# Performance work log

Measured on AMD Instinct MI355X. Metric: run time of the kernel, lower is better.

The kernel has to match this reference:

```python
import jax, jax.numpy as jnp
import numpy as np

EMBED_DIM = 256
NUM_HEADS = 8
HEAD_DIM = EMBED_DIM // NUM_HEADS
WINDOW = 31
B, S = 4, 2048


def _make_params(key):
    ks = jax.random.split(key, 8)
    sc = 0.05
    Wq = jax.random.normal(ks[0], (NUM_HEADS, EMBED_DIM, HEAD_DIM), jnp.float32) * sc
    bq = jax.random.normal(ks[1], (NUM_HEADS, HEAD_DIM), jnp.float32) * sc
    Wk = jax.random.normal(ks[2], (NUM_HEADS, EMBED_DIM, HEAD_DIM), jnp.float32) * sc
    bk = jax.random.normal(ks[3], (NUM_HEADS, HEAD_DIM), jnp.float32) * sc
    Wv = jax.random.normal(ks[4], (NUM_HEADS, EMBED_DIM, HEAD_DIM), jnp.float32) * sc
    bv = jax.random.normal(ks[5], (NUM_HEADS, HEAD_DIM), jnp.float32) * sc
    Wo = jax.random.normal(ks[6], (NUM_HEADS * HEAD_DIM, EMBED_DIM), jnp.float32) * sc
    bo = jax.random.normal(ks[7], (EMBED_DIM,), jnp.float32) * sc
    return Wq, bq, Wk, bk, Wv, bv, Wo, bo


def setup_inputs() -> dict:
    key = jax.random.key(0)
    k1, k2, k3, k4 = jax.random.split(key, 4)
    eeg = jax.random.normal(k1, (B, S, EMBED_DIM), jnp.float32)
    pps = jax.random.normal(k2, (B, S, EMBED_DIM), jnp.float32)
    e2p = _make_params(k3)
    p2e = _make_params(k4)
    names = ["Wq", "bq", "Wk", "bk", "Wv", "bv", "Wo", "bo"]
    inp = {"eeg": eeg, "pps": pps}
    for n, p in zip(names, e2p):
        inp["e2p_" + n] = p
    for n, p in zip(names, p2e):
        inp["p2e_" + n] = p
    return inp


def _cross_window_attn(q_seq, kv_seq, Wq, bq, Wk, bk, Wv, bv, Wo, bo, window):
    # q_seq, kv_seq: [B, S, D]. Each query position i attends to window of
    # the zero-padded kv sequence centered at i (pad positions get bias-only k/v,
    # matching torch Linear applied to zero vectors).
    b, s, d_in = q_seq.shape
    h, _, hd = Wq.shape
    pad = (window - 1) // 2
    kv_pad = jnp.pad(kv_seq, ((0, 0), (pad, pad), (0, 0)))
    Q = jnp.einsum('bsd,hde->bhse', q_seq, Wq) + bq[None, :, None, :]
    K = jnp.einsum('bsd,hde->bhse', kv_pad, Wk) + bk[None, :, None, :]
    V = jnp.einsum('bsd,hde->bhse', kv_pad, Wv) + bv[None, :, None, :]
    idx = jnp.arange(s)[:, None] + jnp.arange(window)[None, :]  # [S, W]
    Kw = K[:, :, idx, :]  # [B, H, S, W, hd]
    Vw = V[:, :, idx, :]
    scores = jnp.einsum('bhse,bhswe->bhsw', Q, Kw) / np.sqrt(hd).astype(np.float32)
    attn = jax.nn.softmax(scores, axis=-1)
    out = jnp.einsum('bhsw,bhswe->bhse', attn, Vw)  # [B, H, S, hd]
    out = out.transpose(0, 2, 1, 3).reshape(b, s, h * hd)
    return out @ Wo + bo


def reference(eeg, pps,
              e2p_Wq, e2p_bq, e2p_Wk, e2p_bk, e2p_Wv, e2p_bv, e2p_Wo, e2p_bo,
              p2e_Wq, p2e_bq, p2e_Wk, p2e_bk, p2e_Wv, p2e_bv, p2e_Wo, p2e_bo):
    fused_eeg = _cross_window_attn(eeg, pps, e2p_Wq, e2p_bq, e2p_Wk, e2p_bk,
                                   e2p_Wv, e2p_bv, e2p_Wo, e2p_bo, WINDOW)
    fused_pps = _cross_window_attn(pps, eeg, p2e_Wq, p2e_bq, p2e_Wk, p2e_bk,
                                   p2e_Wv, p2e_bv, p2e_Wo, p2e_bo, WINDOW)
    return fused_eeg, fused_pps
```

## Files before the change

kernel.cpp:

```cpp
#include <hip/hip_runtime.h>

static __device__ __forceinline__ float bf2f(unsigned short u) {
    return __uint_as_float(((unsigned int)u) << 16);
}
static __device__ __forceinline__ unsigned short f2bf(float f) {
    unsigned int x = __float_as_uint(f);
    unsigned int lsb = (x >> 16) & 1u;
    x += 0x7fffu + lsb;
    return (unsigned short)(x >> 16);
}

typedef __attribute__((ext_vector_type(8))) short short8;
typedef __attribute__((ext_vector_type(4))) float floatx4;

static __device__ __forceinline__ short8 ldg8(const unsigned short* p) {
    short8 v; __builtin_memcpy(&v, p, 16); return v;
}


__global__ __launch_bounds__(256) void repack_kernel(
    const float* e2p_Wq, const float* e2p_bq,
    const float* e2p_Wk, const float* e2p_bk,
    const float* e2p_Wv, const float* e2p_bv,
    const float* e2p_Wo, const float* e2p_bo,
    const float* p2e_Wq, const float* p2e_bq,
    const float* p2e_Wk, const float* p2e_bk,
    const float* p2e_Wv, const float* p2e_bv,
    const float* p2e_Wo, const float* p2e_bo,
    const float* eeg, const float* pps,
    unsigned short* Wpack, unsigned short* Wopack, float* bias_pack, float* bias2,
    unsigned short* Abf)
{
    const int idx = blockIdx.x * 256 + threadIdx.x;

    if (idx < 49152) {
        int inp = idx / 24576, r = idx % 24576;
        int n = r >> 5, k8 = r & 31;
        int kc = k8 >> 2, q4 = k8 & 3, kb = k8 * 8;
        int proj = n / 256, h = (n % 256) / 32, e = n % 32;
        const float* W;
        if (inp == 0) W = (proj == 0) ? e2p_Wq : (proj == 1) ? p2e_Wk : p2e_Wv;
        else          W = (proj == 0) ? p2e_Wq : (proj == 1) ? e2p_Wk : e2p_Wv;
        unsigned short o[8];
        #pragma unroll
        for (int j = 0; j < 8; ++j) o[j] = f2bf(W[h * 8192 + (kb + j) * 32 + e]);
        __builtin_memcpy(Wpack + inp * 196608 + ((n >> 4) * 8 + kc) * 512 + (q4 * 16 + (n & 15)) * 8, o, 16);
    }
    int i2 = idx - 49152;
    if (i2 >= 0 && i2 < 16384) {
        int dir = i2 / 8192, r = i2 % 8192;
        int n = r >> 5, k8 = r & 31;
        int kc = k8 >> 2, q4 = k8 & 3, kb = k8 * 8;
        const float* Wo = dir ? p2e_Wo : e2p_Wo;
        unsigned short o[8];
        #pragma unroll
        for (int j = 0; j < 8; ++j) o[j] = f2bf(Wo[(kb + j) * 256 + n]);
        __builtin_memcpy(Wopack + dir * 65536 + ((n >> 4) * 8 + kc) * 512 + (q4 * 16 + (n & 15)) * 8, o, 16);
    }
    if (idx < 1536) {
        int inp = idx / 768, n = idx % 768;
        int proj = n / 256, he = n % 256;
        const float* bsrc;
        if (inp == 0) bsrc = (proj == 0) ? e2p_bq : (proj == 1) ? p2e_bk : p2e_bv;
        else          bsrc = (proj == 0) ? p2e_bq : (proj == 1) ? e2p_bk : e2p_bv;
        bias_pack[idx] = bsrc[he];
    }
    if (idx >= 1536 && idx < 2048) {
        int j = idx - 1536;
        int dir = j / 256, n = j % 256;
        bias2[j] = (dir == 0 ? e2p_bo : p2e_bo)[n];
    }
    {
        int m_total = idx >> 5;
        int k8 = idx & 31;
        int inp = m_total >> 13, m = m_total & 8191;
        int kc = k8 >> 2, q4 = k8 & 3, kb = k8 * 8;
        const float* src = inp ? pps : eeg;
        float v[8];
        __builtin_memcpy(v, src + (long)m * 256 + kb, 32);
        unsigned short o[8];
        #pragma unroll
        for (int j = 0; j < 8; ++j) o[j] = f2bf(v[j]);
        __builtin_memcpy(Abf + inp * 2097152 + (((m >> 4) * 8 + kc) * 512 + (q4 * 16 + (m & 15)) * 8), o, 16);
    }
}

__global__ __launch_bounds__(256) void mfma_gemm_kernel(
    const unsigned short* __restrict__ A0, const unsigned short* __restrict__ A1,
    const unsigned short* __restrict__ B0f, const unsigned short* __restrict__ B1f,
    const float* __restrict__ bias0, const float* __restrict__ bias1,
    unsigned short* __restrict__ C0, unsigned short* __restrict__ C1,
    int N)
{
    __shared__ __align__(16) unsigned short Cs[128][136];

    const int z = blockIdx.z;
    const unsigned short* A = z ? A1 : A0;
    const unsigned short* Bf = z ? B1f : B0f;
    const float* bias = z ? bias1 : bias0;
    unsigned short* C = z ? C1 : C0;

    const int tid = threadIdx.x;
    const long m0 = (long)blockIdx.x * 128;
    const int n0 = blockIdx.y * 128;

    const int lane = tid & 63;
    const int wv = tid >> 6;
    const int wm = (wv >> 1) * 64, wn = (wv & 1) * 64;
    const int fr = lane & 15, q4 = lane >> 4;

    const unsigned short* Aw = A + ((blockIdx.x * 8 + (wm >> 4)) * 8) * 512 + lane * 8;
    const unsigned short* Bw = Bf + ((blockIdx.y * 8 + (wn >> 4)) * 8) * 512 + lane * 8;

    floatx4 acc[4][4] = {};
    short8 af[2][4], bf_[2][4];

    #pragma unroll
    for (int i = 0; i < 4; ++i) af[0][i] = ldg8(Aw + i * 4096);
    #pragma unroll
    for (int j = 0; j < 4; ++j) bf_[0][j] = ldg8(Bw + j * 4096);

    #pragma unroll
    for (int kc = 0; kc < 8; ++kc) {
        const int cur = kc & 1, nxt = cur ^ 1;
        if (kc < 7) {
            #pragma unroll
            for (int i = 0; i < 4; ++i) af[nxt][i] = ldg8(Aw + (i * 8 + kc + 1) * 512);
            #pragma unroll
            for (int j = 0; j < 4; ++j) bf_[nxt][j] = ldg8(Bw + (j * 8 + kc + 1) * 512);
        }
        #pragma unroll
        for (int i = 0; i < 4; ++i)
            #pragma unroll
            for (int j = 0; j < 4; ++j)
                acc[i][j] = __builtin_amdgcn_mfma_f32_16x16x32_bf16(af[cur][i], bf_[cur][j], acc[i][j], 0, 0, 0);
    }

    float bj[4];
    #pragma unroll
    for (int j = 0; j < 4; ++j) bj[j] = bias[n0 + wn + j * 16 + fr];

    const int cr0 = wm + (q4 << 2);
    #pragma unroll
    for (int i = 0; i < 4; ++i)
        #pragma unroll
        for (int j = 0; j < 4; ++j)
            #pragma unroll
            for (int r = 0; r < 4; ++r)
                Cs[cr0 + i * 16 + r][wn + j * 16 + fr] = f2bf(acc[i][j][r] + bj[j]);
    __syncthreads();

    const int rr = tid >> 4, cc = (tid & 15) * 8;
    #pragma unroll
    for (int p = 0; p < 8; ++p) {
        int r = p * 16 + rr;
        unsigned short tmp[8];
        __builtin_memcpy(tmp, &Cs[r][cc], 16);
        __builtin_memcpy(C + (m0 + r) * N + n0 + cc, tmp, 16);
    }
}

#define KROWS 48
#define VROWS 64
#define KVSTR 264
__global__ __launch_bounds__(512) void attn_out_kernel(
    const unsigned short* __restrict__ Y, const float* __restrict__ bias_pack,
    const unsigned short* __restrict__ Wopack, const float* __restrict__ bias2,
    float* __restrict__ out)
{
    __shared__ unsigned short smem[(KROWS + VROWS) * KVSTR];
    unsigned short* Ks = smem;
    unsigned short* Vs = smem + KROWS * KVSTR;
    unsigned short (*Ps)[16][72] = (unsigned short(*)[16][72])smem;
    unsigned short (*As)[KVSTR] = (unsigned short(*)[KVSTR])smem;

    const int s0 = blockIdx.x * 16;
    const int b = blockIdx.y, dir = blockIdx.z;
    const int kvinp = 1 - dir;
    const int tid = threadIdx.x;

    const float* bkv = bias_pack + kvinp * 768;
    const long kvbase = ((long)kvinp * 8192 + b * 2048) * 768;

    {
        const int r = tid >> 3, seg = (tid & 7) * 32;
        int p = s0 - 15 + r;
        unsigned short vr[32];
        if (p >= 0 && p < 2048) {
            __builtin_memcpy(vr, Y + kvbase + (long)p * 768 + 512 + seg, 64);
        } else {
            #pragma unroll
            for (int j = 0; j < 32; ++j) vr[j] = f2bf(bkv[512 + seg + j]);
        }
        __builtin_memcpy(&Vs[r * KVSTR + seg], vr, 64);
        if (tid < 384) {
            unsigned short kr[32];
            if (p >= 0 && p < 2048) {
                __builtin_memcpy(kr, Y + kvbase + (long)p * 768 + 256 + seg, 64);
            } else {
                #pragma unroll
                for (int j = 0; j < 32; ++j) kr[j] = f2bf(bkv[256 + seg + j]);
            }
            __builtin_memcpy(&Ks[r * KVSTR + seg], kr, 64);
        }
    }

    const int lane = tid & 63;
    const int wv = tid >> 6;
    const int fr = lane & 15, q4 = lane >> 4;
    short8 aq = ldg8(Y + ((long)dir * 8192 + b * 2048 + s0 + fr) * 768 + wv * 32 + q4 * 8);

    __syncthreads();

    floatx4 sacc[3] = {};
    #pragma unroll
    for (int kvt = 0; kvt < 3; ++kvt) {
        short8 bk_ = *(const short8*)&Ks[(kvt * 16 + fr) * KVSTR + wv * 32 + q4 * 8];
        sacc[kvt] = __builtin_amdgcn_mfma_f32_16x16x32_bf16(aq, bk_, sacc[kvt], 0, 0, 0);
    }

    float sv[3][4];
    float mx[4] = {-3.0e38f, -3.0e38f, -3.0e38f, -3.0e38f};
    #pragma unroll
    for (int kvt = 0; kvt < 3; ++kvt)
        #pragma unroll
        for (int reg = 0; reg < 4; ++reg) {
            int i = q4 * 4 + reg;
            int jc = kvt * 16 + fr;
            int d = jc - i;
            float x = (d >= 0 && d <= 30) ? sacc[kvt][reg] * 0.17677669529663687f : -3.0e38f;
            sv[kvt][reg] = x;
            mx[reg] = fmaxf(mx[reg], x);
        }
    #pragma unroll
    for (int off = 1; off < 16; off <<= 1)
        #pragma unroll
        for (int reg = 0; reg < 4; ++reg)
            mx[reg] = fmaxf(mx[reg], __shfl_xor(mx[reg], off));
    float ps[4] = {};
    #pragma unroll
    for (int kvt = 0; kvt < 3; ++kvt)
        #pragma unroll
        for (int reg = 0; reg < 4; ++reg) {
            float e = __expf(sv[kvt][reg] - mx[reg]);
            sv[kvt][reg] = e;
            ps[reg] += e;
        }
    #pragma unroll
    for (int off = 1; off < 16; off <<= 1)
        #pragma unroll
        for (int reg = 0; reg < 4; ++reg)
            ps[reg] += __shfl_xor(ps[reg], off);

    __syncthreads();

    #pragma unroll
    for (int reg = 0; reg < 4; ++reg) {
        int i = q4 * 4 + reg;
        #pragma unroll
        for (int kvt = 0; kvt < 3; ++kvt)
            Ps[wv][i][kvt * 16 + fr] = f2bf(sv[kvt][reg]);
        Ps[wv][i][48 + fr] = 0;
    }

    floatx4 oacc[2] = {};
    #pragma unroll
    for (int ch = 0; ch < 2; ++ch) {
        short8 ap = *(const short8*)&Ps[wv][fr][ch * 32 + q4 * 8];
        #pragma unroll
        for (int et = 0; et < 2; ++et) {
            short8 bv;
            #pragma unroll
            for (int j = 0; j < 8; ++j)
                bv[j] = (short)Vs[(ch * 32 + q4 * 8 + j) * KVSTR + wv * 32 + et * 16 + fr];
            oacc[et] = __builtin_amdgcn_mfma_f32_16x16x32_bf16(ap, bv, oacc[et], 0, 0, 0);
        }
    }

    float rs[4];
    #pragma unroll
    for (int reg = 0; reg < 4; ++reg) rs[reg] = 1.0f / ps[reg];

    __syncthreads();

    #pragma unroll
    for (int et = 0; et < 2; ++et)
        #pragma unroll
        for (int reg = 0; reg < 4; ++reg)
            As[q4 * 4 + reg][wv * 32 + et * 16 + fr] = f2bf(oacc[et][reg] * rs[reg]);

    __syncthreads();

    const unsigned short* Wo = Wopack + dir * 65536 + lane * 8;
    const int nw = wv * 32;
    floatx4 oa[2] = {};
    #pragma unroll
    for (int kc = 0; kc < 8; ++kc) {
        short8 ap = *(const short8*)&As[fr][kc * 32 + q4 * 8];
        #pragma unroll
        for (int j = 0; j < 2; ++j) {
            short8 bw = ldg8(Wo + ((wv * 2 + j) * 8 + kc) * 512);
            oa[j] = __builtin_amdgcn_mfma_f32_16x16x32_bf16(ap, bw, oa[j], 0, 0, 0);
        }
    }

    float bj[2];
    #pragma unroll
    for (int j = 0; j < 2; ++j) bj[j] = bias2[dir * 256 + nw + j * 16 + fr];

    float* outp = out + (long)dir * 2097152;
    #pragma unroll
    for (int j = 0; j < 2; ++j)
        #pragma unroll
        for (int reg = 0; reg < 4; ++reg) {
            int i = q4 * 4 + reg;
            outp[((long)b * 2048 + s0 + i) * 256 + nw + j * 16 + fr] = oa[j][reg] + bj[j];
        }
}

extern "C" void kernel_launch(void* const* d_in, const int* in_sizes, int n_in,
                              void* d_out, int out_size, void* d_ws, size_t ws_size,
                              hipStream_t stream)
{
    float* out = (float*)d_out;

    char* ws = (char*)d_ws;
    unsigned short* Wpack   = (unsigned short*)(ws + 0);
    unsigned short* Wopack  = (unsigned short*)(ws + 786432);
    float*          biasP   = (float*)(ws + 1048576);
    float*          bias2   = (float*)(ws + 1054720);
    unsigned short* Y       = (unsigned short*)(ws + 1056768);
    unsigned short* Abf     = (unsigned short*)(ws + 26222592);

    repack_kernel<<<2048, 256, 0, stream>>>(
        (const float*)d_in[2],  (const float*)d_in[3],
        (const float*)d_in[4],  (const float*)d_in[5],
        (const float*)d_in[6],  (const float*)d_in[7],
        (const float*)d_in[8],  (const float*)d_in[9],
        (const float*)d_in[10], (const float*)d_in[11],
        (const float*)d_in[12], (const float*)d_in[13],
        (const float*)d_in[14], (const float*)d_in[15],
        (const float*)d_in[16], (const float*)d_in[17],
        (const float*)d_in[0],  (const float*)d_in[1],
        Wpack, Wopack, biasP, bias2, Abf);

    mfma_gemm_kernel<<<dim3(64, 6, 2), 256, 0, stream>>>(
        Abf, Abf + 2097152, Wpack, Wpack + 196608, biasP, biasP + 768,
        Y, Y + 8192 * 768, 768);

    attn_out_kernel<<<dim3(128, 4, 2), 512, 0, stream>>>(Y, biasP, Wopack, bias2, out);
}
```

Measured before the change: 140.4 us.

## Coalesce repack and output stores via shared-memory staging and block role split

The repack kernel now assigns dedicated block ranges to each task. The activation conversion stages each 16-row tile through shared memory, so the packed bf16 layout is written as contiguous 16-byte chunks instead of scattered stores. The weight repack index mapping is reordered so consecutive threads write adjacent packed addresses. The attention output epilogue stages the fp32 result tile in shared memory and writes full 32-byte row segments, replacing strided per-element stores, at the cost of extra barriers and shared-memory traffic.

```diff
diff --git a/kernel.cpp b/kernel.cpp
--- a/kernel.cpp
+++ b/kernel.cpp
@@ -31,11 +31,33 @@
     unsigned short* Wpack, unsigned short* Wopack, float* bias_pack, float* bias2,
     unsigned short* Abf)
 {
-    const int idx = blockIdx.x * 256 + threadIdx.x;
-
-    if (idx < 49152) {
+    __shared__ unsigned short tr[2048];
+    const int bid = blockIdx.x, tid = threadIdx.x;
+
+    if (bid < 2048) {
+        const int g = bid >> 1, kc_half = (bid & 1) * 4;
+        const int inp = g >> 9;
+        const int m = (g & 511) * 16 + (tid >> 4);
+        const int k8 = kc_half * 4 + (tid & 15);
+        const float* src = inp ? pps : eeg;
+        float v[8];
+        __builtin_memcpy(v, src + (long)m * 256 + k8 * 8, 32);
+        unsigned short o[8];
+        #pragma unroll
+        for (int j = 0; j < 8; ++j) o[j] = f2bf(v[j]);
+        const int k8l = tid & 15;
+        __builtin_memcpy(&tr[(k8l >> 2) * 512 + ((k8l & 3) * 16 + (tid >> 4)) * 8], o, 16);
+        __syncthreads();
+        unsigned short t[8];
+        __builtin_memcpy(t, &tr[tid * 8], 16);
+        __builtin_memcpy(Abf + inp * 2097152 + ((g & 511) * 8 + kc_half) * 512 + tid * 8, t, 16);
+        return;
+    }
+    if (bid < 2240) {
+        int idx = (bid - 2048) * 256 + tid;
         int inp = idx / 24576, r = idx % 24576;
-        int n = r >> 5, k8 = r & 31;
+        int n = (r & 15) | ((r >> 9) << 4);
+        int k8 = (r >> 4) & 31;
         int kc = k8 >> 2, q4 = k8 & 3, kb = k8 * 8;
         int proj = n / 256, h = (n % 256) / 32, e = n % 32;
         const float* W;
@@ -45,43 +67,35 @@
         #pragma unroll
         for (int j = 0; j < 8; ++j) o[j] = f2bf(W[h * 8192 + (kb + j) * 32 + e]);
         __builtin_memcpy(Wpack + inp * 196608 + ((n >> 4) * 8 + kc) * 512 + (q4 * 16 + (n & 15)) * 8, o, 16);
-    }
-    int i2 = idx - 49152;
-    if (i2 >= 0 && i2 < 16384) {
+        return;
+    }
+    if (bid < 2304) {
+        int i2 = (bid - 2240) * 256 + tid;
         int dir = i2 / 8192, r = i2 % 8192;
-        int n = r >> 5, k8 = r & 31;
+        int n = (r & 15) | ((r >> 9) << 4);
+        int k8 = (r >> 4) & 31;
         int kc = k8 >> 2, q4 = k8 & 3, kb = k8 * 8;
         const float* Wo = dir ? p2e_Wo : e2p_Wo;
         unsigned short o[8];
         #pragma unroll
         for (int j = 0; j < 8; ++j) o[j] = f2bf(Wo[(kb + j) * 256 + n]);
         __builtin_memcpy(Wopack + dir * 65536 + ((n >> 4) * 8 + kc) * 512 + (q4 * 16 + (n & 15)) * 8, o, 16);
-    }
-    if (idx < 1536) {
-        int inp = idx / 768, n = idx % 768;
-        int proj = n / 256, he = n % 256;
-        const float* bsrc;
-        if (inp == 0) bsrc = (proj == 0) ? e2p_bq : (proj == 1) ? p2e_bk : p2e_bv;
-        else          bsrc = (proj == 0) ? p2e_bq : (proj == 1) ? e2p_bk : e2p_bv;
-        bias_pack[idx] = bsrc[he];
-    }
-    if (idx >= 1536 && idx < 2048) {
-        int j = idx - 1536;
-        int dir = j / 256, n = j % 256;
-        bias2[j] = (dir == 0 ? e2p_bo : p2e_bo)[n];
+        return;
     }
     {
-        int m_total = idx >> 5;
-        int k8 = idx & 31;
-        int inp = m_total >> 13, m = m_total & 8191;
-        int kc = k8 >> 2, q4 = k8 & 3, kb = k8 * 8;
-        const float* src = inp ? pps : eeg;
-        float v[8];
-        __builtin_memcpy(v, src + (long)m * 256 + kb, 32);
-        unsigned short o[8];
-        #pragma unroll
-        for (int j = 0; j < 8; ++j) o[j] = f2bf(v[j]);
-        __builtin_memcpy(Abf + inp * 2097152 + (((m >> 4) * 8 + kc) * 512 + (q4 * 16 + (m & 15)) * 8), o, 16);
+        int idx = (bid - 2304) * 256 + tid;
+        if (idx < 1536) {
+            int inp = idx / 768, n = idx % 768;
+            int proj = n / 256, he = n % 256;
+            const float* bsrc;
+            if (inp == 0) bsrc = (proj == 0) ? e2p_bq : (proj == 1) ? p2e_bk : p2e_bv;
+            else          bsrc = (proj == 0) ? p2e_bq : (proj == 1) ? e2p_bk : e2p_bv;
+            bias_pack[idx] = bsrc[he];
+        } else {
+            int j = idx - 1536;
+            int dir = j / 256, n = j % 256;
+            bias2[j] = (dir == 0 ? e2p_bo : p2e_bo)[n];
+        }
     }
 }
 
@@ -168,11 +182,12 @@
     const unsigned short* __restrict__ Wopack, const float* __restrict__ bias2,
     float* __restrict__ out)
 {
-    __shared__ unsigned short smem[(KROWS + VROWS) * KVSTR];
+    __shared__ __align__(16) unsigned short smem[(KROWS + VROWS) * KVSTR];
     unsigned short* Ks = smem;
     unsigned short* Vs = smem + KROWS * KVSTR;
     unsigned short (*Ps)[16][72] = (unsigned short(*)[16][72])smem;
     unsigned short (*As)[KVSTR] = (unsigned short(*)[KVSTR])smem;
+    float (*Os)[264] = (float(*)[264])smem;
 
     const int s0 = blockIdx.x * 16;
     const int b = blockIdx.y, dir = blockIdx.z;
@@ -308,14 +323,20 @@
     #pragma unroll
     for (int j = 0; j < 2; ++j) bj[j] = bias2[dir * 256 + nw + j * 16 + fr];
 
-    float* outp = out + (long)dir * 2097152;
+    __syncthreads();
+
     #pragma unroll
     for (int j = 0; j < 2; ++j)
         #pragma unroll
-        for (int reg = 0; reg < 4; ++reg) {
-            int i = q4 * 4 + reg;
-            outp[((long)b * 2048 + s0 + i) * 256 + nw + j * 16 + fr] = oa[j][reg] + bj[j];
-        }
+        for (int reg = 0; reg < 4; ++reg)
+            Os[q4 * 4 + reg][nw + j * 16 + fr] = oa[j][reg] + bj[j];
+
+    __syncthreads();
+
+    const int row = tid >> 5, col = (tid & 31) * 8;
+    float t8[8];
+    __builtin_memcpy(t8, &Os[row][col], 32);
+    __builtin_memcpy(out + (long)dir * 2097152 + ((long)b * 2048 + s0 + row) * 256 + col, t8, 32);
 }
 
 extern "C" void kernel_launch(void* const* d_in, const int* in_sizes, int n_in,
@@ -332,7 +353,7 @@
     unsigned short* Y       = (unsigned short*)(ws + 1056768);
     unsigned short* Abf     = (unsigned short*)(ws + 26222592);
 
-    repack_kernel<<<2048, 256, 0, stream>>>(
+    repack_kernel<<<2312, 256, 0, stream>>>(
         (const float*)d_in[2],  (const float*)d_in[3],
         (const float*)d_in[4],  (const float*)d_in[5],
         (const float*)d_in[6],  (const float*)d_in[7],
```

Measured after the change: 138.4 us. No clear change (-1.4%).
